# Kernel tuning notes

Measured on AMD Instinct MI355X. Metric: run time of the kernel, lower is better.

Reference implementation:

```python
import jax, jax.numpy as jnp
import numpy as np

HIDDEN = 1024
HEADS = 16
HEAD_DIM = HIDDEN // HEADS  # 64
MAX_SEQ = 2048


def _rope_tables():
    # RotaryEmbedding buffers: freqs_cos/sin of shape [max_seq_len, head_dim//2]
    inv_freq = 1.0 / (10000.0 ** (jnp.arange(0, HEAD_DIM, 2, dtype=jnp.float32) / HEAD_DIM))
    t = jnp.arange(MAX_SEQ, dtype=jnp.float32)
    freqs = t[:, None] * inv_freq[None, :]
    return jnp.cos(freqs), jnp.sin(freqs)


def setup_inputs() -> dict:
    key = jax.random.key(0)
    k1, k2, k3 = jax.random.split(key, 3)
    x = jax.random.normal(k1, (2, 2048, HIDDEN), dtype=jnp.float32)
    qkv_w = jax.random.normal(k2, (HIDDEN, 3 * HIDDEN), dtype=jnp.float32) * 0.02
    qkv_b = jnp.zeros((3 * HIDDEN,), dtype=jnp.float32)
    out_w = jax.random.normal(k3, (HIDDEN, HIDDEN), dtype=jnp.float32) * 0.02
    out_b = jnp.zeros((HIDDEN,), dtype=jnp.float32)
    return {"x": x, "qkv_w": qkv_w, "qkv_b": qkv_b, "out_w": out_w, "out_b": out_b}


def reference(x, qkv_w, qkv_b, out_w, out_b):
    b, s, _ = x.shape
    qkv = x @ qkv_w + qkv_b                                   # [b, s, 3*hidden]
    qkv = qkv.reshape(b, s, HEADS, 3 * HEAD_DIM).transpose(0, 2, 1, 3)  # [b, h, s, 3*hd]
    q, k, v = jnp.split(qkv, 3, axis=-1)                      # each [b, h, s, hd]

    # Faithful to source quirk: rotary() is called on [b, h, s, hd] tensors so
    # x.shape[1] == num_heads -> seq_pos = arange(num_heads); tables are indexed
    # by HEAD index and broadcast over the sequence axis.
    cos_tab, sin_tab = _rope_tables()
    cos = cos_tab[:HEADS][None, :, None, :]                   # [1, h, 1, hd/2]
    sin = sin_tab[:HEADS][None, :, None, :]

    def rot(u):
        u1 = u[..., : HEAD_DIM // 2]
        u2 = u[..., HEAD_DIM // 2 :]
        return jnp.concatenate([u1 * cos - u2 * sin, u2 * cos + u1 * sin], axis=-1)

    q = rot(q)
    k = rot(k)

    scores = jnp.einsum("bhqd,bhkd->bhqk", q, k) / (HEAD_DIM ** 0.5)  # [b, h, s, s]
    attn = jax.nn.softmax(scores.astype(jnp.float32), axis=-1).astype(scores.dtype)
    out = jnp.einsum("bhqk,bhkd->bhqd", attn, v)              # [b, h, s, hd]
    out = out.transpose(0, 2, 1, 3).reshape(b, s, HEADS * HEAD_DIM)
    return out @ out_w + out_b
```

## Files before the change

### kernel.cpp

```cpp
#include <hip/hip_runtime.h>
#include <hip/hip_bf16.h>
#include <cstdint>
#include <cstddef>

typedef float  f32x4  __attribute__((ext_vector_type(4)));
typedef __bf16 bf16x8 __attribute__((ext_vector_type(8)));
typedef __bf16 bf16x4 __attribute__((ext_vector_type(4)));

#define HIDDEN 1024
#define SEQ    2048
#define BATCH  2
#define NQKV   3072
#define MTOT   4096

__device__ __forceinline__ __bf16 f2bf(float f) {
  unsigned u = __builtin_bit_cast(unsigned, f);
  u += 0x7FFFu + ((u >> 16) & 1u);
  unsigned short s = (unsigned short)(u >> 16);
  return __builtin_bit_cast(__bf16, s);
}

__device__ __forceinline__ unsigned pk2(float a, float b) {
  unsigned ua = __builtin_bit_cast(unsigned, a) + 0x8000u;
  unsigned ub = __builtin_bit_cast(unsigned, b) + 0x8000u;
  return __builtin_amdgcn_perm(ub, ua, 0x07060302u);
}

__device__ __forceinline__ float fexp2(float x) {
#if __has_builtin(__builtin_amdgcn_exp2f)
  return __builtin_amdgcn_exp2f(x);
#else
  return exp2f(x);
#endif
}

__device__ __forceinline__ void async16(const void* g, void* l) {
  __builtin_amdgcn_global_load_lds((__attribute__((address_space(1))) void*)(g),
                                   (__attribute__((address_space(3))) void*)(l),
                                   16, 0, 0);
}

__global__ __launch_bounds__(256) void k_prep(const float* __restrict__ x,
                                              __bf16* __restrict__ xb,
                                              const float* __restrict__ qkv_w,
                                              __bf16* __restrict__ wqkT,
                                              const float* __restrict__ out_w,
                                              __bf16* __restrict__ woT) {
  __shared__ float tile[64][65];
  const int bid = blockIdx.x, t = threadIdx.x;
  if (bid < 4096) {
    int i = bid * 256 + t;
    float4 v = ((const float4*)x)[i];
    bf16x4 o;
    o[0] = f2bf(v.x); o[1] = f2bf(v.y); o[2] = f2bf(v.z); o[3] = f2bf(v.w);
    ((bf16x4*)xb)[i] = o;
    return;
  }
  const float* W; __bf16* WT; int N, bx, by;
  if (bid < 4864) { int g = bid - 4096; W = qkv_w; WT = wqkT; N = NQKV;  bx = g % 48; by = g / 48; }
  else            { int g = bid - 4864; W = out_w; WT = woT;  N = HIDDEN; bx = g % 16; by = g / 16; }
  const int K = HIDDEN;
  int tx = t & 63, ty = t >> 6;
  int n0 = bx * 64, k0 = by * 64;
#pragma unroll
  for (int r = 0; r < 16; r++) {
    int row = r * 4 + ty;
    tile[row][tx] = W[(size_t)(k0 + row) * N + n0 + tx];
  }
  __syncthreads();
#pragma unroll
  for (int i2 = 0; i2 < 2; i2++) {
    int cc = i2 * 256 + t;
    int n = cc >> 3, ch = cc & 7;
    bf16x8 o;
#pragma unroll
    for (int j = 0; j < 8; j++) o[j] = f2bf(tile[ch * 8 + j][n]);
    *(bf16x8*)(WT + (size_t)(n0 + n) * K + k0 + ch * 8) = o;
  }
}

template <int BF16OUT, int VFUSE, int TN>
__global__ __launch_bounds__(256, (TN == 64 ? 4 : 3)) void k_gemm(
    const __bf16* __restrict__ A,
    const __bf16* __restrict__ BT,
    const float* __restrict__ bias,
    void* __restrict__ Cout,
    __bf16* __restrict__ vt,
    int M, int N, int K) {
  constexpr int NT = TN / 32;
  __shared__ __align__(16) __bf16 As[2 * 128 * 32];
  __shared__ __align__(16) __bf16 Bs[2 * TN * 32];
  const int t = threadIdx.x;
  const int lane = t & 63, wv = t >> 6;
  const int ln = lane & 15, quad = lane >> 4;
  const int sw8 = (quad ^ ((ln >> 1) & 3)) * 8;
  const int wm = (wv & 1) * 64, wn = (wv >> 1) * (TN / 2);

  const int nbx = N / TN;
  const int cx = nbx >> 1;
  const int lin = blockIdx.x;
  const int xcd = lin & 7, wi = lin >> 3;
  const int bxi = (xcd & 1) * cx + wi % cx;
  const int byi = (xcd >> 1) * 8 + wi / cx;
  const int m0 = byi * 128, n0 = bxi * TN;

  auto stage = [&](int k0, int p) {
    __bf16* Ad = As + p * (128 * 32);
    __bf16* Bd = Bs + p * (TN * 32);
#pragma unroll
    for (int i = 0; i < 2; i++) {
      int tt = i * 256 + t;
      int row = tt >> 2, ch = tt & 3;
      int chs = ch ^ ((row >> 1) & 3);
      async16(A + (size_t)(m0 + row) * K + k0 + chs * 8, Ad + tt * 8);
    }
#pragma unroll
    for (int i = 0; i < TN / 64; i++) {
      int tt = i * 256 + t;
      int row = tt >> 2, ch = tt & 3;
      int chs = ch ^ ((row >> 1) & 3);
      async16(BT + (size_t)(n0 + row) * K + k0 + chs * 8, Bd + tt * 8);
    }
  };

  const f32x4 zero4 = {0.f, 0.f, 0.f, 0.f};
  f32x4 acc[4][NT];
#pragma unroll
  for (int i = 0; i < 4; i++)
#pragma unroll
    for (int j = 0; j < NT; j++) acc[i][j] = zero4;

  stage(0, 0);
  const int NIT = K / 32;
  for (int it = 0; it < NIT; it++) {
    __syncthreads();
    if (it + 1 < NIT) stage((it + 1) * 32, (it + 1) & 1);
    const __bf16* Asb = As + (it & 1) * (128 * 32);
    const __bf16* Bsb = Bs + (it & 1) * (TN * 32);
    bf16x8 af[4], bfr[NT];
#pragma unroll
    for (int x = 0; x < 4; x++)
      af[x] = *(const bf16x8*)(Asb + (wm + x * 16 + ln) * 32 + sw8);
#pragma unroll
    for (int x = 0; x < NT; x++)
      bfr[x] = *(const bf16x8*)(Bsb + (wn + x * 16 + ln) * 32 + sw8);
#pragma unroll
    for (int mt = 0; mt < 4; mt++)
#pragma unroll
      for (int nt = 0; nt < NT; nt++)
        acc[mt][nt] = __builtin_amdgcn_mfma_f32_16x16x32_bf16(af[mt], bfr[nt], acc[mt][nt], 0, 0, 0);
  }
  const float CE = 0.125f * 1.44269504089f;
#pragma unroll
  for (int nt = 0; nt < NT; nt++) {
    int g = n0 + wn + nt * 16;
    int col = g + ln;
    float bv = bias[col];
    int off = g % 192;
    if (!VFUSE || off < 128) {
      float scl = (VFUSE && off < 64) ? CE : 1.0f;
#pragma unroll
      for (int mt = 0; mt < 4; mt++) {
#pragma unroll
        for (int r = 0; r < 4; r++) {
          int row = m0 + wm + mt * 16 + quad * 4 + r;
          float v = (acc[mt][nt][r] + bv) * scl;
          if (BF16OUT) ((__bf16*)Cout)[(size_t)row * N + col] = f2bf(v);
          else         ((float*)Cout)[(size_t)row * N + col] = v;
        }
      }
    } else {
      int hg = g / 192;
      int d  = off - 128 + ln;
#pragma unroll
      for (int mt = 0; mt < 4; mt++) {
        int rowb = m0 + wm + mt * 16;
        int bb = rowb >> 11;
        int s  = rowb & 2047;
        int sblk = s >> 7;
        int blk  = (s >> 4) & 7;
        int p = (blk & 3) * 32 + quad * 8 + ((blk >> 2) << 2);
        uint2 o;
        o.x = pk2(acc[mt][nt][0] + bv, acc[mt][nt][1] + bv);
        o.y = pk2(acc[mt][nt][2] + bv, acc[mt][nt][3] + bv);
        *(uint2*)(vt + ((size_t)((bb * 16 + hg) * 64 + d)) * SEQ + sblk * 128 + p) = o;
      }
    }
  }
}

__global__ __launch_bounds__(512, 4) void k_attn(const __bf16* __restrict__ qkv,
                                                 const __bf16* __restrict__ vt,
                                                 __bf16* __restrict__ aout) {
  __shared__ __align__(16) __bf16 smem[32768];
  const int t = threadIdx.x;
  const int lane = t & 63, wv = t >> 6;
  const int ln = lane & 15, quad = lane >> 4;
  const int sw8 = (quad ^ ((ln >> 1) & 3)) * 8;

  int gid = blockIdx.x;
  int slot = gid & 7, j = gid >> 3;
  int bh = slot * 4 + (j >> 4);
  int qt0 = j & 15;
  const int b = bh >> 4, h = bh & 15;
  const int q0 = qt0 * 128;

  const __bf16* qbase = qkv + (size_t)b * SEQ * NQKV + h * 192;
  const __bf16* kbase = qbase + 64;
  const __bf16* vbase = vt + (size_t)bh * 64 * SEQ;

#pragma unroll
  for (int i = 0; i < 2; i++) {
    int tt = i * 512 + t;
    int hh = tt >> 9, row = (tt >> 2) & 127, ch = tt & 3;
    int chs = ch ^ ((row >> 1) & 3);
    async16(kbase + (size_t)row * NQKV + hh * 32 + chs * 8, smem + tt * 8);
  }
#pragma unroll
  for (int i = 0; i < 2; i++) {
    int tt = i * 512 + t;
    int c = tt >> 8, d = (tt >> 2) & 63, w = tt & 3;
    int ws = w ^ ((d >> 1) & 3);
    async16(vbase + (size_t)d * SEQ + c * 32 + ws * 8, smem + 16384 + tt * 8);
  }

  bf16x8 qf[2];
#pragma unroll
  for (int dc = 0; dc < 2; dc++)
    qf[dc] = *(const bf16x8*)(qbase + (size_t)(q0 + wv * 16 + ln) * NQKV + dc * 32 + quad * 8);

  union { unsigned u[4]; bf16x8 v; } ones;
  ones.u[0] = ones.u[1] = ones.u[2] = ones.u[3] = 0x3F803F80u;

  const f32x4 zero4 = {0.f, 0.f, 0.f, 0.f};
  f32x4 O[4];
  f32x4 Ol = zero4;
#pragma unroll
  for (int dt = 0; dt < 4; dt++) O[dt] = zero4;

  for (int it = 0; it < SEQ / 128; it++) {
    __syncthreads();
    const __bf16* Ks = smem + (it & 1) * 8192;
    const __bf16* Vs = smem + 16384 + (it & 1) * 8192;
    if (it + 1 < SEQ / 128) {
      __bf16* Kd = smem + ((it + 1) & 1) * 8192;
      __bf16* Vd = smem + 16384 + ((it + 1) & 1) * 8192;
      const __bf16* kn = kbase + (size_t)(it + 1) * 128 * NQKV;
      const __bf16* vn = vbase + (it + 1) * 128;
#pragma unroll
      for (int i = 0; i < 2; i++) {
        int tt = i * 512 + t;
        int hh = tt >> 9, row = (tt >> 2) & 127, ch = tt & 3;
        int chs = ch ^ ((row >> 1) & 3);
        async16(kn + (size_t)row * NQKV + hh * 32 + chs * 8, Kd + tt * 8);
      }
#pragma unroll
      for (int i = 0; i < 2; i++) {
        int tt = i * 512 + t;
        int c = tt >> 8, d = (tt >> 2) & 63, w = tt & 3;
        int ws = w ^ ((d >> 1) & 3);
        async16(vn + (size_t)d * SEQ + c * 32 + ws * 8, Vd + tt * 8);
      }
    }

    unsigned Pp[8][2];
#pragma unroll
    for (int blk = 0; blk < 8; blk++) {
      bf16x8 kf0 = *(const bf16x8*)(Ks +        (blk * 16 + ln) * 32 + sw8);
      bf16x8 kf1 = *(const bf16x8*)(Ks + 4096 + (blk * 16 + ln) * 32 + sw8);
      f32x4 s = __builtin_amdgcn_mfma_f32_16x16x32_bf16(kf0, qf[0], zero4, 0, 0, 0);
      s = __builtin_amdgcn_mfma_f32_16x16x32_bf16(kf1, qf[1], s, 0, 0, 0);
      Pp[blk][0] = pk2(fexp2(s[0]), fexp2(s[1]));
      Pp[blk][1] = pk2(fexp2(s[2]), fexp2(s[3]));
    }
#pragma unroll
    for (int kc = 0; kc < 4; kc++) {
      union { bf16x8 v; unsigned u[4]; } pf;
      pf.u[0] = Pp[kc][0]; pf.u[1] = Pp[kc][1];
      pf.u[2] = Pp[kc + 4][0]; pf.u[3] = Pp[kc + 4][1];
      Ol = __builtin_amdgcn_mfma_f32_16x16x32_bf16(pf.v, ones.v, Ol, 0, 0, 0);
#pragma unroll
      for (int dt = 0; dt < 4; dt++) {
        bf16x8 vf = *(const bf16x8*)(Vs + kc * 2048 + (dt * 16 + ln) * 32 + sw8);
        O[dt] = __builtin_amdgcn_mfma_f32_16x16x32_bf16(pf.v, vf, O[dt], 0, 0, 0);
      }
    }
  }

  __bf16* stage = smem + wv * 1024;
#pragma unroll
  for (int r = 0; r < 4; r++) {
    float ir = 1.0f / Ol[r];
#pragma unroll
    for (int dt = 0; dt < 4; dt++)
      stage[(quad * 4 + r) * 64 + dt * 16 + ln] = f2bf(O[dt][r] * ir);
  }
  __bf16* obase = aout + (size_t)(b * SEQ + q0 + wv * 16) * HIDDEN + h * 64;
#pragma unroll
  for (int i = 0; i < 2; i++) {
    int tt = i * 64 + lane; int row = tt >> 3, ch = tt & 7;
    *(bf16x8*)(obase + (size_t)row * HIDDEN + ch * 8) = *(const bf16x8*)(stage + row * 64 + ch * 8);
  }
}

extern "C" void kernel_launch(void* const* d_in, const int* in_sizes, int n_in,
                              void* d_out, int out_size, void* d_ws, size_t ws_size,
                              hipStream_t stream) {
  const float* x     = (const float*)d_in[0];
  const float* qkv_w = (const float*)d_in[1];
  const float* qkv_b = (const float*)d_in[2];
  const float* out_w = (const float*)d_in[3];
  const float* out_b = (const float*)d_in[4];

  char* ws = (char*)d_ws;
  __bf16* xb   = (__bf16*)(ws);
  __bf16* wqkT = (__bf16*)(ws + 8388608);
  __bf16* woT  = (__bf16*)(ws + 14680064);
  __bf16* qkv  = (__bf16*)(ws + 16777216);
  __bf16* vt   = (__bf16*)(ws + 41943040);
  __bf16* aout = (__bf16*)(ws + 50331648);

  k_prep<<<5120, 256, 0, stream>>>(x, xb, qkv_w, wqkT, out_w, woT);
  k_gemm<1, 1, 128><<<768, 256, 0, stream>>>(xb, wqkT, qkv_b, qkv, vt, MTOT, NQKV, HIDDEN);
  k_attn<<<512, 512, 0, stream>>>(qkv, vt, aout);
  k_gemm<0, 0, 64><<<512, 256, 0, stream>>>(aout, woT, out_b, (float*)d_out, nullptr, MTOT, HIDDEN, HIDDEN);
}
```

Before: 176.0 us.

## Use 256x256 tiles with 4-stage pipeline for QKV GEMM; add MFMA priority hints

The QKV projection moves to a dedicated kernel with 256x256 block tiles, 512 threads and a 4-deep async LDS ring buffer that uses explicit vmcnt waits, so each loaded byte gets more reuse and memory latency is hidden across stages. The output GEMM becomes its own non-templated copy with unchanged behaviour. The attention kernel wraps its MFMA sections in s_setprio to favour matrix issue over other waves. The trade-off is that the grid drops to 192 blocks, fewer than the CU count, so some CUs sit idle, and the larger LDS and register footprint lowers occupancy.

```diff
diff --git a/kernel.cpp b/kernel.cpp
--- a/kernel.cpp
+++ b/kernel.cpp
@@ -79,44 +79,39 @@
   }
 }
 
-template <int BF16OUT, int VFUSE, int TN>
-__global__ __launch_bounds__(256, (TN == 64 ? 4 : 3)) void k_gemm(
-    const __bf16* __restrict__ A,
-    const __bf16* __restrict__ BT,
-    const float* __restrict__ bias,
-    void* __restrict__ Cout,
-    __bf16* __restrict__ vt,
-    int M, int N, int K) {
-  constexpr int NT = TN / 32;
-  __shared__ __align__(16) __bf16 As[2 * 128 * 32];
-  __shared__ __align__(16) __bf16 Bs[2 * TN * 32];
+__global__ __launch_bounds__(512, 2) void k_qkv(const __bf16* __restrict__ A,
+                                                const __bf16* __restrict__ BT,
+                                                const float* __restrict__ bias,
+                                                __bf16* __restrict__ Cout,
+                                                __bf16* __restrict__ vt) {
+  const int K = HIDDEN;
+  __shared__ __align__(16) __bf16 As[4][256 * 32];
+  __shared__ __align__(16) __bf16 Bs[4][256 * 32];
   const int t = threadIdx.x;
   const int lane = t & 63, wv = t >> 6;
   const int ln = lane & 15, quad = lane >> 4;
   const int sw8 = (quad ^ ((ln >> 1) & 3)) * 8;
-  const int wm = (wv & 1) * 64, wn = (wv >> 1) * (TN / 2);
-
-  const int nbx = N / TN;
-  const int cx = nbx >> 1;
+  const int wm = (wv >> 2) * 128, wn = (wv & 3) * 64;
+
   const int lin = blockIdx.x;
   const int xcd = lin & 7, wi = lin >> 3;
-  const int bxi = (xcd & 1) * cx + wi % cx;
-  const int byi = (xcd >> 1) * 8 + wi / cx;
-  const int m0 = byi * 128, n0 = bxi * TN;
+  const int bxi = (xcd & 3) * 3 + wi % 3;
+  const int byi = (xcd >> 2) * 8 + wi / 3;
+  const int m0 = byi * 256, n0 = bxi * 256;
 
   auto stage = [&](int k0, int p) {
-    __bf16* Ad = As + p * (128 * 32);
-    __bf16* Bd = Bs + p * (TN * 32);
+    __bf16* Ad = As[p];
+    __bf16* Bd = Bs[p];
 #pragma unroll
     for (int i = 0; i < 2; i++) {
-      int tt = i * 256 + t;
+      int tt = i * 512 + t;
       int row = tt >> 2, ch = tt & 3;
       int chs = ch ^ ((row >> 1) & 3);
       async16(A + (size_t)(m0 + row) * K + k0 + chs * 8, Ad + tt * 8);
     }
 #pragma unroll
-    for (int i = 0; i < TN / 64; i++) {
-      int tt = i * 256 + t;
+    for (int i = 0; i < 2; i++) {
+      int tt = i * 512 + t;
       int row = tt >> 2, ch = tt & 3;
       int chs = ch ^ ((row >> 1) & 3);
       async16(BT + (size_t)(n0 + row) * K + k0 + chs * 8, Bd + tt * 8);
@@ -124,56 +119,58 @@
   };
 
   const f32x4 zero4 = {0.f, 0.f, 0.f, 0.f};
-  f32x4 acc[4][NT];
-#pragma unroll
-  for (int i = 0; i < 4; i++)
-#pragma unroll
-    for (int j = 0; j < NT; j++) acc[i][j] = zero4;
-
-  stage(0, 0);
+  f32x4 acc[8][4];
+#pragma unroll
+  for (int i = 0; i < 8; i++)
+#pragma unroll
+    for (int j = 0; j < 4; j++) acc[i][j] = zero4;
+
+  stage(0, 0); stage(32, 1); stage(64, 2);
   const int NIT = K / 32;
-  for (int it = 0; it < NIT; it++) {
-    __syncthreads();
-    if (it + 1 < NIT) stage((it + 1) * 32, (it + 1) & 1);
-    const __bf16* Asb = As + (it & 1) * (128 * 32);
-    const __bf16* Bsb = Bs + (it & 1) * (TN * 32);
-    bf16x8 af[4], bfr[NT];
+  for (int j = 0; j < NIT; j++) {
+    int rem = NIT - 1 - j;
+    if (rem >= 2)      asm volatile("s_waitcnt vmcnt(8)\n\ts_barrier" ::: "memory");
+    else if (rem == 1) asm volatile("s_waitcnt vmcnt(4)\n\ts_barrier" ::: "memory");
+    else               asm volatile("s_waitcnt vmcnt(0)\n\ts_barrier" ::: "memory");
+    if (j + 3 < NIT) stage((j + 3) * 32, (j + 3) & 3);
+    const __bf16* Asb = As[j & 3];
+    const __bf16* Bsb = Bs[j & 3];
+    bf16x8 af[8], bfr[4];
+#pragma unroll
+    for (int x = 0; x < 8; x++)
+      af[x] = *(const bf16x8*)(Asb + (wm + x * 16 + ln) * 32 + sw8);
 #pragma unroll
     for (int x = 0; x < 4; x++)
-      af[x] = *(const bf16x8*)(Asb + (wm + x * 16 + ln) * 32 + sw8);
-#pragma unroll
-    for (int x = 0; x < NT; x++)
       bfr[x] = *(const bf16x8*)(Bsb + (wn + x * 16 + ln) * 32 + sw8);
 #pragma unroll
-    for (int mt = 0; mt < 4; mt++)
-#pragma unroll
-      for (int nt = 0; nt < NT; nt++)
+    for (int mt = 0; mt < 8; mt++)
+#pragma unroll
+      for (int nt = 0; nt < 4; nt++)
         acc[mt][nt] = __builtin_amdgcn_mfma_f32_16x16x32_bf16(af[mt], bfr[nt], acc[mt][nt], 0, 0, 0);
   }
+
   const float CE = 0.125f * 1.44269504089f;
 #pragma unroll
-  for (int nt = 0; nt < NT; nt++) {
+  for (int nt = 0; nt < 4; nt++) {
     int g = n0 + wn + nt * 16;
     int col = g + ln;
     float bv = bias[col];
     int off = g % 192;
-    if (!VFUSE || off < 128) {
-      float scl = (VFUSE && off < 64) ? CE : 1.0f;
-#pragma unroll
-      for (int mt = 0; mt < 4; mt++) {
+    if (off < 128) {
+      float scl = (off < 64) ? CE : 1.0f;
+#pragma unroll
+      for (int mt = 0; mt < 8; mt++) {
 #pragma unroll
         for (int r = 0; r < 4; r++) {
           int row = m0 + wm + mt * 16 + quad * 4 + r;
-          float v = (acc[mt][nt][r] + bv) * scl;
-          if (BF16OUT) ((__bf16*)Cout)[(size_t)row * N + col] = f2bf(v);
-          else         ((float*)Cout)[(size_t)row * N + col] = v;
+          Cout[(size_t)row * NQKV + col] = f2bf((acc[mt][nt][r] + bv) * scl);
         }
       }
     } else {
       int hg = g / 192;
       int d  = off - 128 + ln;
 #pragma unroll
-      for (int mt = 0; mt < 4; mt++) {
+      for (int mt = 0; mt < 8; mt++) {
         int rowb = m0 + wm + mt * 16;
         int bb = rowb >> 11;
         int s  = rowb & 2047;
@@ -189,6 +186,88 @@
   }
 }
 
+__global__ __launch_bounds__(256, 4) void k_gemm_out(const __bf16* __restrict__ A,
+                                                     const __bf16* __restrict__ BT,
+                                                     const float* __restrict__ bias,
+                                                     float* __restrict__ Cout,
+                                                     int M, int N, int K) {
+  constexpr int TN = 64;
+  __shared__ __align__(16) __bf16 As[2 * 128 * 32];
+  __shared__ __align__(16) __bf16 Bs[2 * TN * 32];
+  const int t = threadIdx.x;
+  const int lane = t & 63, wv = t >> 6;
+  const int ln = lane & 15, quad = lane >> 4;
+  const int sw8 = (quad ^ ((ln >> 1) & 3)) * 8;
+  const int wm = (wv & 1) * 64, wn = (wv >> 1) * (TN / 2);
+
+  const int nbx = N / TN;
+  const int cx = nbx >> 1;
+  const int lin = blockIdx.x;
+  const int xcd = lin & 7, wi = lin >> 3;
+  const int bxi = (xcd & 1) * cx + wi % cx;
+  const int byi = (xcd >> 1) * 8 + wi / cx;
+  const int m0 = byi * 128, n0 = bxi * TN;
+
+  auto stage = [&](int k0, int p) {
+    __bf16* Ad = As + p * (128 * 32);
+    __bf16* Bd = Bs + p * (TN * 32);
+#pragma unroll
+    for (int i = 0; i < 2; i++) {
+      int tt = i * 256 + t;
+      int row = tt >> 2, ch = tt & 3;
+      int chs = ch ^ ((row >> 1) & 3);
+      async16(A + (size_t)(m0 + row) * K + k0 + chs * 8, Ad + tt * 8);
+    }
+    {
+      int tt = t;
+      int row = tt >> 2, ch = tt & 3;
+      int chs = ch ^ ((row >> 1) & 3);
+      async16(BT + (size_t)(n0 + row) * K + k0 + chs * 8, Bd + tt * 8);
+    }
+  };
+
+  const f32x4 zero4 = {0.f, 0.f, 0.f, 0.f};
+  f32x4 acc[4][2];
+#pragma unroll
+  for (int i = 0; i < 4; i++)
+#pragma unroll
+    for (int j = 0; j < 2; j++) acc[i][j] = zero4;
+
+  stage(0, 0);
+  const int NIT = K / 32;
+  for (int it = 0; it < NIT; it++) {
+    __syncthreads();
+    if (it + 1 < NIT) stage((it + 1) * 32, (it + 1) & 1);
+    const __bf16* Asb = As + (it & 1) * (128 * 32);
+    const __bf16* Bsb = Bs + (it & 1) * (TN * 32);
+    bf16x8 af[4], bfr[2];
+#pragma unroll
+    for (int x = 0; x < 4; x++)
+      af[x] = *(const bf16x8*)(Asb + (wm + x * 16 + ln) * 32 + sw8);
+#pragma unroll
+    for (int x = 0; x < 2; x++)
+      bfr[x] = *(const bf16x8*)(Bsb + (wn + x * 16 + ln) * 32 + sw8);
+#pragma unroll
+    for (int mt = 0; mt < 4; mt++)
+#pragma unroll
+      for (int nt = 0; nt < 2; nt++)
+        acc[mt][nt] = __builtin_amdgcn_mfma_f32_16x16x32_bf16(af[mt], bfr[nt], acc[mt][nt], 0, 0, 0);
+  }
+#pragma unroll
+  for (int nt = 0; nt < 2; nt++) {
+    int col = n0 + wn + nt * 16 + ln;
+    float bv = bias[col];
+#pragma unroll
+    for (int mt = 0; mt < 4; mt++) {
+#pragma unroll
+      for (int r = 0; r < 4; r++) {
+        int row = m0 + wm + mt * 16 + quad * 4 + r;
+        Cout[(size_t)row * N + col] = acc[mt][nt][r] + bv;
+      }
+    }
+  }
+}
+
 __global__ __launch_bounds__(512, 4) void k_attn(const __bf16* __restrict__ qkv,
                                                  const __bf16* __restrict__ vt,
                                                  __bf16* __restrict__ aout) {
@@ -268,8 +347,10 @@
     for (int blk = 0; blk < 8; blk++) {
       bf16x8 kf0 = *(const bf16x8*)(Ks +        (blk * 16 + ln) * 32 + sw8);
       bf16x8 kf1 = *(const bf16x8*)(Ks + 4096 + (blk * 16 + ln) * 32 + sw8);
+      __builtin_amdgcn_s_setprio(1);
       f32x4 s = __builtin_amdgcn_mfma_f32_16x16x32_bf16(kf0, qf[0], zero4, 0, 0, 0);
       s = __builtin_amdgcn_mfma_f32_16x16x32_bf16(kf1, qf[1], s, 0, 0, 0);
+      __builtin_amdgcn_s_setprio(0);
       Pp[blk][0] = pk2(fexp2(s[0]), fexp2(s[1]));
       Pp[blk][1] = pk2(fexp2(s[2]), fexp2(s[3]));
     }
@@ -278,12 +359,14 @@
       union { bf16x8 v; unsigned u[4]; } pf;
       pf.u[0] = Pp[kc][0]; pf.u[1] = Pp[kc][1];
       pf.u[2] = Pp[kc + 4][0]; pf.u[3] = Pp[kc + 4][1];
+      __builtin_amdgcn_s_setprio(1);
       Ol = __builtin_amdgcn_mfma_f32_16x16x32_bf16(pf.v, ones.v, Ol, 0, 0, 0);
 #pragma unroll
       for (int dt = 0; dt < 4; dt++) {
         bf16x8 vf = *(const bf16x8*)(Vs + kc * 2048 + (dt * 16 + ln) * 32 + sw8);
         O[dt] = __builtin_amdgcn_mfma_f32_16x16x32_bf16(pf.v, vf, O[dt], 0, 0, 0);
       }
+      __builtin_amdgcn_s_setprio(0);
     }
   }
 
@@ -321,7 +404,7 @@
   __bf16* aout = (__bf16*)(ws + 50331648);
 
   k_prep<<<5120, 256, 0, stream>>>(x, xb, qkv_w, wqkT, out_w, woT);
-  k_gemm<1, 1, 128><<<768, 256, 0, stream>>>(xb, wqkT, qkv_b, qkv, vt, MTOT, NQKV, HIDDEN);
+  k_qkv<<<192, 512, 0, stream>>>(xb, wqkT, qkv_b, qkv, vt);
   k_attn<<<512, 512, 0, stream>>>(qkv, vt, aout);
-  k_gemm<0, 0, 64><<<512, 256, 0, stream>>>(aout, woT, out_b, (float*)d_out, nullptr, MTOT, HIDDEN, HIDDEN);
-}
+  k_gemm_out<<<512, 256, 0, stream>>>(aout, woT, out_b, (float*)d_out, MTOT, HIDDEN, HIDDEN);
+}
```

Result: slower. 188.1 us (+6.9%).
